# Performance work log

Hardware: AMD Instinct MI355X
Metric: run time of the kernel (lower is better)

## Reference

```python
import jax, jax.numpy as jnp
import numpy as np

SIM_THRESHOLD = 0.5   # similarity_threshold
LAMBDA = 0.1          # lambda_weight default


def setup_inputs() -> dict:
    key = jax.random.key(0)
    ks = jax.random.split(key, 8)
    B, T, C, P = 8, 1024, 1024, 100
    return {
        "attention_scores": jax.random.normal(ks[0], (B, T, T), jnp.float32),
        "context": jax.random.normal(ks[1], (B, C), jnp.float32),
        "triggers": jax.random.normal(ks[2], (P, C), jnp.float32),
        "biases": jax.random.uniform(ks[3], (P, T, T), jnp.float32),
        "confidences": jnp.ones((P,), jnp.float32),
        "W1": jax.random.normal(ks[4], (2 * C, C), jnp.float32) * (1.0 / np.sqrt(2 * C)),
        "b1": jnp.zeros((C,), jnp.float32),
        "W2": jax.random.normal(ks[5], (C,), jnp.float32) * (1.0 / np.sqrt(C)),
        "b2": jnp.zeros((1,), jnp.float32),
    }


def reference(attention_scores, context, triggers, biases, confidences, W1, b1, W2, b2):
    C = context.shape[-1]
    # combined = cat([context, trigger]) @ W1 == context @ W1[:C] + trigger @ W1[C:]
    ctx_h = context @ W1[:C]              # (B, C)
    trg_h = triggers @ W1[C:]             # (P, C)
    h = jax.nn.relu(ctx_h[:, None, :] + trg_h[None, :, :] + b1)   # (B, P, C)
    logits = h @ W2 + b2[0]               # (B, P)
    scores = jax.nn.sigmoid(logits).mean(axis=0)                  # (P,) mean over batch
    # match: only patterns with score > threshold contribute, weighted by score*confidence
    weights = jnp.where(scores > SIM_THRESHOLD, scores * confidences, 0.0)  # (P,)
    reasoning_bias = jnp.einsum("p,pij->ij", weights, biases)     # (T, T)
    return attention_scores + LAMBDA * reasoning_bias[None, :, :]
```

## Files before the change

kernel.cpp:

```cpp
#include <hip/hip_runtime.h>
#include <hip/hip_bf16.h>
#include <math.h>

#define BD 8
#define TD 1024
#define CD 1024
#define PD 100
#define KS 8
#define KW (CD / KS)
#define LAMBDA 0.1f
#define SIM_THR 0.5f

__device__ float g_pctx[KS][BD][CD];
__device__ float g_ptrg[KS][PD][CD];
__device__ float g_wd[PD];

__global__ __launch_bounds__(256) void hidden_kernel(const float* __restrict__ context,
                                                     const float* __restrict__ triggers,
                                                     const float* __restrict__ W1) {
    const int c  = blockIdx.x * 256 + threadIdx.x;
    const int kz = blockIdx.z;
    const int k0 = kz * KW;
    const bool is_ctx = (blockIdx.y == 0);
    const int  ych = blockIdx.y - 1;
    const float* __restrict__ W1p = is_ctx ? W1 : (W1 + (size_t)CD * CD);
    const float* __restrict__ src = is_ctx ? context : (triggers + (size_t)ych * 10 * CD);
    float* __restrict__ dst = is_ctx ? &g_pctx[kz][0][0] : &g_ptrg[kz][ych * 10][0];
    const int nrows = is_ctx ? 8 : 10;

    __shared__ float s_src[10][KW];
    for (int t = threadIdx.x; t < 10 * KW; t += 256) {
        const int r = t / KW, k = t % KW;
        s_src[r][k] = src[(size_t)(r < nrows ? r : 0) * CD + k0 + k];
    }
    __syncthreads();

    float acc[10];
#pragma unroll
    for (int i = 0; i < 10; ++i) acc[i] = 0.f;

#pragma unroll 8
    for (int kk = 0; kk < KW; ++kk) {
        const float wv = W1p[(size_t)(k0 + kk) * CD + c];
#pragma unroll
        for (int i = 0; i < 10; ++i)
            acc[i] = fmaf(s_src[i][kk], wv, acc[i]);
    }
#pragma unroll
    for (int i = 0; i < 10; ++i)
        if (i < nrows) dst[(size_t)i * CD + c] = acc[i];
}

__global__ __launch_bounds__(256) void score_kernel(const float* __restrict__ b1,
                                                    const float* __restrict__ W2,
                                                    const float* __restrict__ b2,
                                                    const float* __restrict__ conf) {
    const int p = blockIdx.x;
    __shared__ float s_h[CD];
    __shared__ float s_logit[BD];

    for (int c = threadIdx.x; c < CD; c += 256) {
        float v = b1[c];
#pragma unroll
        for (int kz = 0; kz < KS; ++kz) v += g_ptrg[kz][p][c];
        s_h[c] = v;
    }
    __syncthreads();

    const int wave = threadIdx.x >> 6, lane = threadIdx.x & 63;
#pragma unroll
    for (int bb = 0; bb < 2; ++bb) {
        const int b = wave * 2 + bb;
        float sum = 0.f;
        for (int c = lane; c < CD; c += 64) {
            float v = s_h[c];
#pragma unroll
            for (int kz = 0; kz < KS; ++kz) v += g_pctx[kz][b][c];
            sum = fmaf(fmaxf(v, 0.f), W2[c], sum);
        }
#pragma unroll
        for (int off = 32; off > 0; off >>= 1) sum += __shfl_down(sum, off);
        if (lane == 0) s_logit[b] = sum + b2[0];
    }
    __syncthreads();
    if (threadIdx.x == 0) {
        float s = 0.f;
#pragma unroll
        for (int b = 0; b < BD; ++b) s += 1.f / (1.f + expf(-s_logit[b]));
        s *= (1.f / BD);
        g_wd[p] = (s > SIM_THR) ? s * conf[p] * LAMBDA : 0.f;
    }
}

__global__ __launch_bounds__(256) void out_kernel(const float* __restrict__ attn,
                                                  const float* __restrict__ biases,
                                                  float* __restrict__ out) {
    __shared__ float s_w[PD];
    __shared__ int   s_idx[PD];
    __shared__ int   s_n;
    if (threadIdx.x < PD) s_w[threadIdx.x] = g_wd[threadIdx.x];
    __syncthreads();
    if (threadIdx.x == 0) {
        int n = 0;
        for (int q = 0; q < PD; ++q)
            if (s_w[q] != 0.f) { s_idx[n] = q; s_w[n] = s_w[q]; ++n; }
        s_n = n;
    }
    __syncthreads();
    const int n = s_n;

    const size_t baseA = (size_t)blockIdx.x * 2048 + (size_t)threadIdx.x * 4;
    const size_t baseB = baseA + 1024;

    float4 aA = make_float4(0.f, 0.f, 0.f, 0.f);
    float4 aB = make_float4(0.f, 0.f, 0.f, 0.f);

    int t = 0;
    for (; t + 2 <= n; t += 2) {
        const float w0 = s_w[t], w1 = s_w[t + 1];
        const float* p0 = biases + (size_t)s_idx[t]     * (TD * TD);
        const float* p1 = biases + (size_t)s_idx[t + 1] * (TD * TD);
        const float4 v0A = *(const float4*)(p0 + baseA);
        const float4 v0B = *(const float4*)(p0 + baseB);
        const float4 v1A = *(const float4*)(p1 + baseA);
        const float4 v1B = *(const float4*)(p1 + baseB);
        aA.x = fmaf(w0, v0A.x, fmaf(w1, v1A.x, aA.x));
        aA.y = fmaf(w0, v0A.y, fmaf(w1, v1A.y, aA.y));
        aA.z = fmaf(w0, v0A.z, fmaf(w1, v1A.z, aA.z));
        aA.w = fmaf(w0, v0A.w, fmaf(w1, v1A.w, aA.w));
        aB.x = fmaf(w0, v0B.x, fmaf(w1, v1B.x, aB.x));
        aB.y = fmaf(w0, v0B.y, fmaf(w1, v1B.y, aB.y));
        aB.z = fmaf(w0, v0B.z, fmaf(w1, v1B.z, aB.z));
        aB.w = fmaf(w0, v0B.w, fmaf(w1, v1B.w, aB.w));
    }
    if (t < n) {
        const float w = s_w[t];
        const float* p0 = biases + (size_t)s_idx[t] * (TD * TD);
        const float4 vA = *(const float4*)(p0 + baseA);
        const float4 vB = *(const float4*)(p0 + baseB);
        aA.x = fmaf(w, vA.x, aA.x); aA.y = fmaf(w, vA.y, aA.y);
        aA.z = fmaf(w, vA.z, aA.z); aA.w = fmaf(w, vA.w, aA.w);
        aB.x = fmaf(w, vB.x, aB.x); aB.y = fmaf(w, vB.y, aB.y);
        aB.z = fmaf(w, vB.z, aB.z); aB.w = fmaf(w, vB.w, aB.w);
    }

#pragma unroll
    for (int b = 0; b < BD; ++b) {
        const size_t offA = (size_t)b * TD * TD + baseA;
        const size_t offB = (size_t)b * TD * TD + baseB;
        const float4 avA = *(const float4*)(attn + offA);
        const float4 avB = *(const float4*)(attn + offB);
        float4 oA, oB;
        oA.x = avA.x + aA.x; oA.y = avA.y + aA.y; oA.z = avA.z + aA.z; oA.w = avA.w + aA.w;
        oB.x = avB.x + aB.x; oB.y = avB.y + aB.y; oB.z = avB.z + aB.z; oB.w = avB.w + aB.w;
        *(float4*)(out + offA) = oA;
        *(float4*)(out + offB) = oB;
    }
}

extern "C" void kernel_launch(void* const* d_in, const int* in_sizes, int n_in,
                              void* d_out, int out_size, void* d_ws, size_t ws_size,
                              hipStream_t stream) {
    const float* attn     = (const float*)d_in[0];
    const float* context  = (const float*)d_in[1];
    const float* triggers = (const float*)d_in[2];
    const float* biases   = (const float*)d_in[3];
    const float* conf     = (const float*)d_in[4];
    const float* W1       = (const float*)d_in[5];
    const float* b1       = (const float*)d_in[6];
    const float* W2       = (const float*)d_in[7];
    const float* b2       = (const float*)d_in[8];
    float* out = (float*)d_out;

    hipLaunchKernelGGL(hidden_kernel, dim3(CD / 256, 11, KS), dim3(256), 0, stream,
                       context, triggers, W1);
    hipLaunchKernelGGL(score_kernel, dim3(PD), dim3(256), 0, stream, b1, W2, b2, conf);
    hipLaunchKernelGGL(out_kernel, dim3(TD / 2), dim3(256), 0, stream, attn, biases, out);
}
```

Baseline: 107.9 us.

## Retune split-K, widen score blocks, unroll bias loads with nontemporal access

The K-split of the hidden projection is doubled to 16 and the score kernel now uses 512 threads, one wave per batch row. The output kernel processes one row per block across 1024 blocks. It issues eight independent float4 bias loads per iteration to raise memory-level parallelism, and uses nontemporal loads and stores for the streamed bias and attention data. The trade-offs are more partial sums to reduce in the score kernel and reliance on the nontemporal cache hints paying off for streaming traffic.

```diff
diff --git a/kernel.cpp b/kernel.cpp
--- a/kernel.cpp
+++ b/kernel.cpp
@@ -6,10 +6,12 @@
 #define TD 1024
 #define CD 1024
 #define PD 100
-#define KS 8
+#define KS 16
 #define KW (CD / KS)
 #define LAMBDA 0.1f
 #define SIM_THR 0.5f
+
+typedef float f4 __attribute__((ext_vector_type(4)));
 
 __device__ float g_pctx[KS][BD][CD];
 __device__ float g_ptrg[KS][PD][CD];
@@ -30,7 +32,7 @@
 
     __shared__ float s_src[10][KW];
     for (int t = threadIdx.x; t < 10 * KW; t += 256) {
-        const int r = t / KW, k = t % KW;
+        const int r = t >> 6, k = t & (KW - 1);
         s_src[r][k] = src[(size_t)(r < nrows ? r : 0) * CD + k0 + k];
     }
     __syncthreads();
@@ -51,7 +53,7 @@
         if (i < nrows) dst[(size_t)i * CD + c] = acc[i];
 }
 
-__global__ __launch_bounds__(256) void score_kernel(const float* __restrict__ b1,
+__global__ __launch_bounds__(512) void score_kernel(const float* __restrict__ b1,
                                                     const float* __restrict__ W2,
                                                     const float* __restrict__ b2,
                                                     const float* __restrict__ conf) {
@@ -59,7 +61,7 @@
     __shared__ float s_h[CD];
     __shared__ float s_logit[BD];
 
-    for (int c = threadIdx.x; c < CD; c += 256) {
+    for (int c = threadIdx.x; c < CD; c += 512) {
         float v = b1[c];
 #pragma unroll
         for (int kz = 0; kz < KS; ++kz) v += g_ptrg[kz][p][c];
@@ -67,26 +69,22 @@
     }
     __syncthreads();
 
-    const int wave = threadIdx.x >> 6, lane = threadIdx.x & 63;
+    const int b = threadIdx.x >> 6, lane = threadIdx.x & 63;
+    float sum = 0.f;
+    for (int c = lane; c < CD; c += 64) {
+        float v = s_h[c];
 #pragma unroll
-    for (int bb = 0; bb < 2; ++bb) {
-        const int b = wave * 2 + bb;
-        float sum = 0.f;
-        for (int c = lane; c < CD; c += 64) {
-            float v = s_h[c];
+        for (int kz = 0; kz < KS; ++kz) v += g_pctx[kz][b][c];
+        sum = fmaf(fmaxf(v, 0.f), W2[c], sum);
+    }
 #pragma unroll
-            for (int kz = 0; kz < KS; ++kz) v += g_pctx[kz][b][c];
-            sum = fmaf(fmaxf(v, 0.f), W2[c], sum);
-        }
-#pragma unroll
-        for (int off = 32; off > 0; off >>= 1) sum += __shfl_down(sum, off);
-        if (lane == 0) s_logit[b] = sum + b2[0];
-    }
+    for (int off = 32; off > 0; off >>= 1) sum += __shfl_down(sum, off);
+    if (lane == 0) s_logit[b] = sum + b2[0];
     __syncthreads();
     if (threadIdx.x == 0) {
         float s = 0.f;
 #pragma unroll
-        for (int b = 0; b < BD; ++b) s += 1.f / (1.f + expf(-s_logit[b]));
+        for (int bb = 0; bb < BD; ++bb) s += 1.f / (1.f + expf(-s_logit[bb]));
         s *= (1.f / BD);
         g_wd[p] = (s > SIM_THR) ? s * conf[p] * LAMBDA : 0.f;
     }
@@ -96,65 +94,64 @@
                                                   const float* __restrict__ biases,
                                                   float* __restrict__ out) {
     __shared__ float s_w[PD];
-    __shared__ int   s_idx[PD];
-    __shared__ int   s_n;
+    __shared__ unsigned long long s_off[PD];
+    __shared__ int s_n;
     if (threadIdx.x < PD) s_w[threadIdx.x] = g_wd[threadIdx.x];
     __syncthreads();
     if (threadIdx.x == 0) {
         int n = 0;
         for (int q = 0; q < PD; ++q)
-            if (s_w[q] != 0.f) { s_idx[n] = q; s_w[n] = s_w[q]; ++n; }
+            if (s_w[q] != 0.f) {
+                s_w[n] = s_w[q];
+                s_off[n] = (unsigned long long)q * (TD * TD);
+                ++n;
+            }
         s_n = n;
     }
     __syncthreads();
     const int n = s_n;
 
-    const size_t baseA = (size_t)blockIdx.x * 2048 + (size_t)threadIdx.x * 4;
-    const size_t baseB = baseA + 1024;
-
-    float4 aA = make_float4(0.f, 0.f, 0.f, 0.f);
-    float4 aB = make_float4(0.f, 0.f, 0.f, 0.f);
+    const size_t rowoff = (size_t)blockIdx.x * TD + (size_t)threadIdx.x * 4;
+    f4 acc = {0.f, 0.f, 0.f, 0.f};
 
     int t = 0;
-    for (; t + 2 <= n; t += 2) {
-        const float w0 = s_w[t], w1 = s_w[t + 1];
-        const float* p0 = biases + (size_t)s_idx[t]     * (TD * TD);
-        const float* p1 = biases + (size_t)s_idx[t + 1] * (TD * TD);
-        const float4 v0A = *(const float4*)(p0 + baseA);
-        const float4 v0B = *(const float4*)(p0 + baseB);
-        const float4 v1A = *(const float4*)(p1 + baseA);
-        const float4 v1B = *(const float4*)(p1 + baseB);
-        aA.x = fmaf(w0, v0A.x, fmaf(w1, v1A.x, aA.x));
-        aA.y = fmaf(w0, v0A.y, fmaf(w1, v1A.y, aA.y));
-        aA.z = fmaf(w0, v0A.z, fmaf(w1, v1A.z, aA.z));
-        aA.w = fmaf(w0, v0A.w, fmaf(w1, v1A.w, aA.w));
-        aB.x = fmaf(w0, v0B.x, fmaf(w1, v1B.x, aB.x));
-        aB.y = fmaf(w0, v0B.y, fmaf(w1, v1B.y, aB.y));
-        aB.z = fmaf(w0, v0B.z, fmaf(w1, v1B.z, aB.z));
-        aB.w = fmaf(w0, v0B.w, fmaf(w1, v1B.w, aB.w));
+    for (; t + 8 <= n; t += 8) {
+        float w[8];
+        const f4* p[8];
+#pragma unroll
+        for (int u = 0; u < 8; ++u) {
+            w[u] = s_w[t + u];
+            p[u] = (const f4*)(biases + (size_t)s_off[t + u] + rowoff);
+        }
+        f4 v[8];
+#pragma unroll
+        for (int u = 0; u < 8; ++u) v[u] = __builtin_nontemporal_load(p[u]);
+#pragma unroll
+        for (int u = 0; u < 8; ++u) {
+            acc.x = fmaf(w[u], v[u].x, acc.x);
+            acc.y = fmaf(w[u], v[u].y, acc.y);
+            acc.z = fmaf(w[u], v[u].z, acc.z);
+            acc.w = fmaf(w[u], v[u].w, acc.w);
+        }
     }
-    if (t < n) {
+    for (; t < n; ++t) {
         const float w = s_w[t];
-        const float* p0 = biases + (size_t)s_idx[t] * (TD * TD);
-        const float4 vA = *(const float4*)(p0 + baseA);
-        const float4 vB = *(const float4*)(p0 + baseB);
-        aA.x = fmaf(w, vA.x, aA.x); aA.y = fmaf(w, vA.y, aA.y);
-        aA.z = fmaf(w, vA.z, aA.z); aA.w = fmaf(w, vA.w, aA.w);
-        aB.x = fmaf(w, vB.x, aB.x); aB.y = fmaf(w, vB.y, aB.y);
-        aB.z = fmaf(w, vB.z, aB.z); aB.w = fmaf(w, vB.w, aB.w);
+        const f4 bv = __builtin_nontemporal_load(
+            (const f4*)(biases + (size_t)s_off[t] + rowoff));
+        acc.x = fmaf(w, bv.x, acc.x);
+        acc.y = fmaf(w, bv.y, acc.y);
+        acc.z = fmaf(w, bv.z, acc.z);
+        acc.w = fmaf(w, bv.w, acc.w);
     }
 
+    f4 av[BD];
+#pragma unroll
+    for (int b = 0; b < BD; ++b)
+        av[b] = __builtin_nontemporal_load((const f4*)(attn + (size_t)b * TD * TD + rowoff));
 #pragma unroll
     for (int b = 0; b < BD; ++b) {
-        const size_t offA = (size_t)b * TD * TD + baseA;
-        const size_t offB = (size_t)b * TD * TD + baseB;
-        const float4 avA = *(const float4*)(attn + offA);
-        const float4 avB = *(const float4*)(attn + offB);
-        float4 oA, oB;
-        oA.x = avA.x + aA.x; oA.y = avA.y + aA.y; oA.z = avA.z + aA.z; oA.w = avA.w + aA.w;
-        oB.x = avB.x + aB.x; oB.y = avB.y + aB.y; oB.z = avB.z + aB.z; oB.w = avB.w + aB.w;
-        *(float4*)(out + offA) = oA;
-        *(float4*)(out + offB) = oB;
+        f4 ov = av[b] + acc;
+        __builtin_nontemporal_store(ov, (f4*)(out + (size_t)b * TD * TD + rowoff));
     }
 }
 
@@ -174,6 +171,6 @@
 
     hipLaunchKernelGGL(hidden_kernel, dim3(CD / 256, 11, KS), dim3(256), 0, stream,
                        context, triggers, W1);
-    hipLaunchKernelGGL(score_kernel, dim3(PD), dim3(256), 0, stream, b1, W2, b2, conf);
-    hipLaunchKernelGGL(out_kernel, dim3(TD / 2), dim3(256), 0, stream, attn, biases, out);
+    hipLaunchKernelGGL(score_kernel, dim3(PD), dim3(512), 0, stream, b1, W2, b2, conf);
+    hipLaunchKernelGGL(out_kernel, dim3(TD), dim3(256), 0, stream, attn, biases, out);
 }
```

New measurement: 105.6 us. -2.1%, faster.
